# Kernel tuning notes

Measured on AMD Instinct MI355X. Metric: run time of the kernel, lower is better.

The kernel has to match this reference:

```python
import jax, jax.numpy as jnp
import numpy as np

B, S, Hd = 2, 2048, 2048
NH, DH = 16, 128
FF = 4 * Hd
EPS = 1e-5


def layer_norm(x, g, b):
    mu = jnp.mean(x, axis=-1, keepdims=True)
    var = jnp.mean(jnp.square(x - mu), axis=-1, keepdims=True)
    return (x - mu) * jax.lax.rsqrt(var + EPS) * g + b


def setup_inputs() -> dict:
    key = jax.random.key(0)
    ks = jax.random.split(key, 10)
    s = lambda n: 1.0 / np.sqrt(n)
    return {
        "hidden_states": jax.random.normal(ks[0], (B, S, Hd), jnp.float32),
        "attention_mask": jnp.zeros((B, S), jnp.float32),
        "ln1_g": jnp.ones((Hd,), jnp.float32),
        "ln1_b": jnp.zeros((Hd,), jnp.float32),
        "ln2_g": jnp.ones((Hd,), jnp.float32),
        "ln2_b": jnp.zeros((Hd,), jnp.float32),
        "Wq": jax.random.normal(ks[1], (Hd, NH * DH), jnp.float32) * s(Hd),
        "Wk": jax.random.normal(ks[2], (Hd, NH * DH), jnp.float32) * s(Hd),
        "Wv": jax.random.normal(ks[3], (Hd, NH * DH), jnp.float32) * s(Hd),
        "Wo": jax.random.normal(ks[4], (NH * DH, Hd), jnp.float32) * s(NH * DH),
        "W1": jax.random.normal(ks[5], (Hd, FF), jnp.float32) * s(Hd),
        "b1": jnp.zeros((FF,), jnp.float32),
        "W2": jax.random.normal(ks[6], (FF, Hd), jnp.float32) * s(FF),
        "b2": jnp.zeros((Hd,), jnp.float32),
    }


def reference(hidden_states, attention_mask, ln1_g, ln1_b, ln2_g, ln2_b,
              Wq, Wk, Wv, Wo, W1, b1, W2, b2):
    x = hidden_states
    # --- attention sub-block ---
    h = layer_norm(x, ln1_g, ln1_b)
    q = (h @ Wq).reshape(B, S, NH, DH)
    k = (h @ Wk).reshape(B, S, NH, DH)
    v = (h @ Wv).reshape(B, S, NH, DH)
    scores = jnp.einsum("bqhd,bkhd->bhqk", q, k) / np.sqrt(DH).astype(np.float32)
    scores = scores + attention_mask[:, None, None, :]  # additive mask
    probs = jax.nn.softmax(scores, axis=-1)
    ctx = jnp.einsum("bhqk,bkhd->bqhd", probs, v).reshape(B, S, NH * DH)
    x = x + ctx @ Wo
    # --- MLP sub-block ---
    h = layer_norm(x, ln2_g, ln2_b)
    h = jax.nn.gelu(h @ W1 + b1, approximate=False)
    x = x + h @ W2 + b2
    return x
```

## Files before the change

### kernel.cpp

```cpp
#include <hip/hip_runtime.h>
#include <math.h>

#define B_ 2
#define S_ 2048
#define HD 2048
#define NH_ 16
#define DH_ 128
#define FF_ 8192
#define MROWS (B_*S_)
#define LDQ 6144

typedef __attribute__((ext_vector_type(8))) short bf16x8;
typedef __attribute__((ext_vector_type(4))) short s16x4;
typedef __attribute__((ext_vector_type(4))) float f32x4;

static __device__ __forceinline__ unsigned short f2bf(float f) {
    unsigned u = __float_as_uint(f);
    u += 0x7fffu + ((u >> 16) & 1u);
    return (unsigned short)(u >> 16);
}

static __device__ __forceinline__ void gload_lds16(const void* g, void* lds) {
    __builtin_amdgcn_global_load_lds((const __attribute__((address_space(1))) void*)g,
                                     (__attribute__((address_space(3))) void*)lds, 16, 0, 0);
}

__global__ __launch_bounds__(256) void trcvt_kernel(const float* __restrict__ W,
        short* __restrict__ Wt, int K, int N) {
    __shared__ float tile[32][33];
    int t = threadIdx.x;
    int tx = t & 31, ty = t >> 5;
    int r0 = blockIdx.y * 32, c0 = blockIdx.x * 32;
    #pragma unroll
    for (int i = 0; i < 4; i++)
        tile[ty + 8*i][tx] = W[(size_t)(r0 + ty + 8*i) * N + c0 + tx];
    __syncthreads();
    #pragma unroll
    for (int i = 0; i < 4; i++)
        Wt[(size_t)(c0 + ty + 8*i) * K + r0 + tx] = (short)f2bf(tile[tx][ty + 8*i]);
}

__global__ __launch_bounds__(256) void vtrans_kernel(const short* __restrict__ qkv,
        short* __restrict__ vT) {
    __shared__ short tile[32][33];
    int t = threadIdx.x;
    int tx = t & 31, ty = t >> 5;
    int c0 = blockIdx.x * 32;
    int r0 = blockIdx.y * 32;
    int b  = blockIdx.z;
    #pragma unroll
    for (int i = 0; i < 4; i++)
        tile[ty + 8*i][tx] = qkv[(size_t)(b*S_ + r0 + ty + 8*i) * LDQ + 4096 + c0 + tx];
    __syncthreads();
    #pragma unroll
    for (int i = 0; i < 4; i++)
        vT[((size_t)(c0 + ty + 8*i) * 2 + b) * S_ + r0 + tx] = tile[tx][ty + 8*i];
}

__global__ __launch_bounds__(256) void ln_kernel(const float* __restrict__ x,
                const float* __restrict__ g, const float* __restrict__ b,
                short* __restrict__ out) {
    int row = blockIdx.x;
    const float* xr = x + (size_t)row * HD;
    short* orow = out + (size_t)row * HD;
    int t = threadIdx.x;

    float4 v0 = ((const float4*)xr)[t];
    float4 v1 = ((const float4*)xr)[t + 256];
    float s  = v0.x + v0.y + v0.z + v0.w + v1.x + v1.y + v1.z + v1.w;
    float ss = v0.x*v0.x + v0.y*v0.y + v0.z*v0.z + v0.w*v0.w
             + v1.x*v1.x + v1.y*v1.y + v1.z*v1.z + v1.w*v1.w;

    #pragma unroll
    for (int off = 1; off < 64; off <<= 1) {
        s  += __shfl_xor(s,  off, 64);
        ss += __shfl_xor(ss, off, 64);
    }
    __shared__ float ws_s[4], ws_q[4];
    int wid = t >> 6;
    if ((t & 63) == 0) { ws_s[wid] = s; ws_q[wid] = ss; }
    __syncthreads();
    s  = ws_s[0] + ws_s[1] + ws_s[2] + ws_s[3];
    ss = ws_q[0] + ws_q[1] + ws_q[2] + ws_q[3];

    float mu  = s * (1.0f / HD);
    float var = ss * (1.0f / HD) - mu * mu;
    float rs  = rsqrtf(var + 1e-5f);

    float4 g0 = ((const float4*)g)[t];
    float4 g1 = ((const float4*)g)[t + 256];
    float4 b0 = ((const float4*)b)[t];
    float4 b1 = ((const float4*)b)[t + 256];
    s16x4 o0, o1;
    o0.x = (short)f2bf((v0.x - mu) * rs * g0.x + b0.x);
    o0.y = (short)f2bf((v0.y - mu) * rs * g0.y + b0.y);
    o0.z = (short)f2bf((v0.z - mu) * rs * g0.z + b0.z);
    o0.w = (short)f2bf((v0.w - mu) * rs * g0.w + b0.w);
    o1.x = (short)f2bf((v1.x - mu) * rs * g1.x + b1.x);
    o1.y = (short)f2bf((v1.y - mu) * rs * g1.y + b1.y);
    o1.z = (short)f2bf((v1.z - mu) * rs * g1.z + b1.z);
    o1.w = (short)f2bf((v1.w - mu) * rs * g1.w + b1.w);
    ((s16x4*)orow)[t]       = o0;
    ((s16x4*)orow)[t + 256] = o1;
}

#define CKPRO() { if constexpr (BM == 256) asm volatile("s_waitcnt vmcnt(4)" ::: "memory"); \
                  else                     asm volatile("s_waitcnt vmcnt(3)" ::: "memory"); }
#define CKLOOP() { if constexpr (BM == 256) asm volatile("s_waitcnt vmcnt(8)" ::: "memory"); \
                   else                     asm volatile("s_waitcnt vmcnt(6)" ::: "memory"); }

#define GPH(BUF, KK, STG) {                                                       \
    bf16x8 av[MFR];                                                               \
    _Pragma("unroll") for (int f = 0; f < MFR; f++)                               \
        av[f] = *(const bf16x8*)(pA + (BUF)*ABUF + (KK)*AKK + f*1024);            \
    bf16x8 bv[4];                                                                 \
    _Pragma("unroll") for (int n = 0; n < 4; n++)                                 \
        bv[n] = *(const bf16x8*)(pB + (BUF)*BBUF + (KK)*BKK + n*1024);            \
    STG;                                                                          \
    CKLOOP();                                                                     \
    __builtin_amdgcn_s_barrier();                                                 \
    __builtin_amdgcn_s_setprio(1);                                                \
    _Pragma("unroll") for (int f = 0; f < MFR; f++)                               \
        _Pragma("unroll") for (int n = 0; n < 4; n++)                             \
            acc[f][n] = __builtin_amdgcn_mfma_f32_16x16x32_bf16(                  \
                av[f], bv[n], acc[f][n], 0, 0, 0);                                \
    __builtin_amdgcn_s_setprio(0);                                                \
    __builtin_amdgcn_s_barrier();                                                 \
}

template<int BM, bool OUTBF16, bool BIAS, bool RES, bool GELU>
__global__ __launch_bounds__(512, 2) void gemm256(
        const short* __restrict__ A, const short* __restrict__ Bt,
        const float* __restrict__ bias, const float* __restrict__ res,
        void* __restrict__ Cout, int M, int N, int K) {
    constexpr int MFR  = BM / 32;
    constexpr int LA   = BM / 128;
    constexpr int AKK  = BM * 64;
    constexpr int ABUF = 2 * AKK;
    constexpr int BKK  = 256 * 64;
    constexpr int BBUF = 2 * BKK;
    __shared__ __align__(16) char ldsA[2 * ABUF];
    __shared__ __align__(16) char ldsB[2 * BBUF];

    int tid = threadIdx.x;
    int wave = tid >> 6, lane = tid & 63;
    int l4 = lane >> 4, lm = lane & 15;
    int wm = wave >> 2, wn = wave & 3;

    int nx = N >> 8;
    int bid = blockIdx.x;
    int m0, n0;
    if constexpr (BM == 128) {
        int xcd = bid & 7, local = bid >> 3;
        int mt = (xcd & 3) * 8 + (local >> 2);
        int ntt = (xcd >> 2) * 4 + (local & 3);
        m0 = mt * 128; n0 = ntt << 8;
    } else {
        m0 = (bid / nx) * BM; n0 = (bid % nx) << 8;
    }

    const short* Atile = A + (size_t)m0 * K;
    const short* Btile = Bt + (size_t)n0 * K;
    const int NT = K >> 6;

    int slot = (l4 ^ (lm & 3) ^ (lm >> 2)) & 3;
    const char* pA = ldsA + (wm * (BM/2) + lm) * 64 + slot * 16;
    const char* pB = ldsB + (wn * 64 + lm) * 64 + slot * 16;

    auto stageA = [&](int t, int kh, int buf) {
        int tw = (t >= NT) ? t - NT : t;
        const short* g = Atile + tw * 64 + kh * 32;
        char* dst = ldsA + buf * ABUF + kh * AKK;
        #pragma unroll
        for (int s = 0; s < LA; s++) {
            int n = wave * (64 * LA) + s * 64 + lane;
            int row = n >> 2, c = n & 3;
            int cs = (c ^ (row & 3) ^ ((row >> 2) & 3)) & 3;
            gload_lds16(g + (size_t)row * K + cs * 8, dst + n * 16);
        }
    };
    auto stageB = [&](int t, int kh, int buf) {
        int tw = (t >= NT) ? t - NT : t;
        const short* g = Btile + tw * 64 + kh * 32;
        char* dst = ldsB + buf * BBUF + kh * BKK;
        #pragma unroll
        for (int s = 0; s < 2; s++) {
            int n = wave * 128 + s * 64 + lane;
            int row = n >> 2, c = n & 3;
            int cs = (c ^ (row & 3) ^ ((row >> 2) & 3)) & 3;
            gload_lds16(g + (size_t)row * K + cs * 8, dst + n * 16);
        }
    };

    f32x4 acc[MFR][4] = {};

    stageA(0, 0, 0); stageB(0, 0, 0);
    stageA(0, 1, 0); stageB(0, 1, 0);
    stageA(1, 0, 1); stageB(1, 0, 1);
    CKPRO();
    __builtin_amdgcn_s_barrier();

    const int NITER = NT >> 1;
    for (int j = 0; j < NITER; j++) {
        int T = 2 * j;
        GPH(0, 0, { stageA(T+1, 1, 1); stageB(T+1, 1, 1); });
        GPH(0, 1, { stageA(T+2, 0, 0); stageB(T+2, 0, 0); });
        GPH(1, 0, { stageA(T+2, 1, 0); stageB(T+2, 1, 0); });
        GPH(1, 1, { stageA(T+3, 0, 1); stageB(T+3, 0, 1); });
    }
    asm volatile("s_waitcnt vmcnt(0)" ::: "memory");
    __builtin_amdgcn_s_barrier();

    #pragma unroll
    for (int n = 0; n < 4; n++) {
        int colb = n0 + wn * 64 + n * 16 + lm;
        float bvs = BIAS ? bias[colb] : 0.f;
        #pragma unroll
        for (int m = 0; m < MFR; m++) {
            #pragma unroll
            for (int r = 0; r < 4; r++) {
                int row = m0 + wm * (BM/2) + m * 16 + l4 * 4 + r;
                float v = acc[m][n][r] + bvs;
                if (GELU) v = 0.5f * v * (1.0f + erff(v * 0.70710678118654752f));
                size_t off = (size_t)row * N + colb;
                if (RES) v += res[off];
                if (OUTBF16) ((short*)Cout)[off] = (short)f2bf(v);
                else         ((float*)Cout)[off] = v;
            }
        }
    }
}

__global__ __launch_bounds__(256) void attn_kernel(
        const short* __restrict__ qkv, const short* __restrict__ vT,
        const float* __restrict__ mask, short* __restrict__ ctx) {
    __shared__ __align__(16) short Ks[64*128];
    __shared__ __align__(16) short Vt[128*64];
    __shared__ __align__(16) short Ps[4][16*72];
    int t = threadIdx.x;
    int wave = t >> 6, lane = t & 63;
    int l4 = lane >> 4, lm = lane & 15;
    int q0 = blockIdx.x * 64, h = blockIdx.y, zb = blockIdx.z;
    const float scale = 0.08838834764831845f;

    bf16x8 aq[4];
    {
        const short* qrow = qkv + (size_t)(zb*S_ + q0 + wave*16 + lm) * LDQ + h*DH_;
        #pragma unroll
        for (int ks = 0; ks < 4; ks++)
            aq[ks] = *(const bf16x8*)(qrow + ks*32 + l4*8);
    }

    float m_r[4], l_r[4];
    #pragma unroll
    for (int r = 0; r < 4; r++) { m_r[r] = -INFINITY; l_r[r] = 0.f; }
    f32x4 o[8];
    #pragma unroll
    for (int i = 0; i < 8; i++) o[i] = (f32x4){0.f, 0.f, 0.f, 0.f};

    for (int kv0 = 0; kv0 < S_; kv0 += 64) {
        __syncthreads();
        #pragma unroll
        for (int L = 0; L < 4; L++) {
            int c = (wave*4 + L)*64 + lane;
            int krow = c >> 4, kc = c & 15;
            int ksrc = (kc & 8) | ((kc ^ (krow & 7)) & 7);
            gload_lds16(qkv + (size_t)(zb*S_ + kv0 + krow)*LDQ + 2048 + h*DH_ + ksrc*8,
                        (char*)Ks + c*16);
            int drow = c >> 3, dc = c & 7;
            int dsrc = dc ^ (drow & 7);
            gload_lds16(vT + ((size_t)(h*DH_ + drow)*2 + zb)*S_ + kv0 + dsrc*8,
                        (char*)Vt + c*16);
        }
        __syncthreads();

        f32x4 s[4];
        #pragma unroll
        for (int nb = 0; nb < 4; nb++) s[nb] = (f32x4){0.f, 0.f, 0.f, 0.f};
        __builtin_amdgcn_s_setprio(1);
        #pragma unroll
        for (int nb = 0; nb < 4; nb++) {
            int row = nb*16 + lm;
            #pragma unroll
            for (int ks = 0; ks < 4; ks++) {
                bf16x8 bk = *(const bf16x8*)((const char*)Ks +
                              ((row*256 + ks*64 + l4*16) ^ ((row & 7) << 4)));
                s[nb] = __builtin_amdgcn_mfma_f32_16x16x32_bf16(aq[ks], bk, s[nb], 0, 0, 0);
            }
        }
        __builtin_amdgcn_s_setprio(0);

        float mk[4];
        #pragma unroll
        for (int nb = 0; nb < 4; nb++) mk[nb] = mask[(size_t)zb*S_ + kv0 + nb*16 + lm];

        float pv_[4][4], fac[4];
        #pragma unroll
        for (int r = 0; r < 4; r++) {
            float vmax = -INFINITY;
            #pragma unroll
            for (int nb = 0; nb < 4; nb++) {
                float v = s[nb][r] * scale + mk[nb];
                pv_[r][nb] = v;
                vmax = fmaxf(vmax, v);
            }
            vmax = fmaxf(vmax, __shfl_xor(vmax, 1, 64));
            vmax = fmaxf(vmax, __shfl_xor(vmax, 2, 64));
            vmax = fmaxf(vmax, __shfl_xor(vmax, 4, 64));
            vmax = fmaxf(vmax, __shfl_xor(vmax, 8, 64));
            float nm = fmaxf(m_r[r], vmax);
            fac[r] = __expf(m_r[r] - nm);
            float ps = 0.f;
            #pragma unroll
            for (int nb = 0; nb < 4; nb++) {
                float e = __expf(pv_[r][nb] - nm);
                pv_[r][nb] = e;
                ps += e;
            }
            ps += __shfl_xor(ps, 1, 64);
            ps += __shfl_xor(ps, 2, 64);
            ps += __shfl_xor(ps, 4, 64);
            ps += __shfl_xor(ps, 8, 64);
            l_r[r] = l_r[r] * fac[r] + ps;
            m_r[r] = nm;
        }
        #pragma unroll
        for (int i = 0; i < 8; i++)
            #pragma unroll
            for (int r = 0; r < 4; r++) o[i][r] *= fac[r];

        short* Pw = (short*)Ps[wave];
        #pragma unroll
        for (int r = 0; r < 4; r++)
            #pragma unroll
            for (int nb = 0; nb < 4; nb++)
                Pw[(l4*4 + r)*72 + nb*16 + lm] = (short)f2bf(pv_[r][nb]);

        __builtin_amdgcn_s_setprio(1);
        #pragma unroll
        for (int ks = 0; ks < 2; ks++) {
            bf16x8 ap = *(const bf16x8*)(Pw + lm*72 + ks*32 + l4*8);
            #pragma unroll
            for (int nd = 0; nd < 8; nd++) {
                int d = nd*16 + lm;
                bf16x8 bvv = *(const bf16x8*)((const char*)Vt +
                              (((d*128) + ks*64 + l4*16) ^ ((d & 7) << 4)));
                o[nd] = __builtin_amdgcn_mfma_f32_16x16x32_bf16(ap, bvv, o[nd], 0, 0, 0);
            }
        }
        __builtin_amdgcn_s_setprio(0);
    }

    float inv[4];
    #pragma unroll
    for (int r = 0; r < 4; r++) inv[r] = 1.0f / l_r[r];
    #pragma unroll
    for (int nd = 0; nd < 8; nd++) {
        #pragma unroll
        for (int r = 0; r < 4; r++) {
            size_t row = (size_t)(zb*S_ + q0 + wave*16 + l4*4 + r);
            ctx[row * HD + h*DH_ + nd*16 + lm] = (short)f2bf(o[nd][r] * inv[r]);
        }
    }
}

extern "C" void kernel_launch(void* const* d_in, const int* in_sizes, int n_in,
                              void* d_out, int out_size, void* d_ws, size_t ws_size,
                              hipStream_t stream) {
    const float* x      = (const float*)d_in[0];
    const float* mask   = (const float*)d_in[1];
    const float* ln1_g  = (const float*)d_in[2];
    const float* ln1_b  = (const float*)d_in[3];
    const float* ln2_g  = (const float*)d_in[4];
    const float* ln2_b  = (const float*)d_in[5];
    const float* Wq     = (const float*)d_in[6];
    const float* Wk     = (const float*)d_in[7];
    const float* Wv     = (const float*)d_in[8];
    const float* Wo     = (const float*)d_in[9];
    const float* W1     = (const float*)d_in[10];
    const float* b1     = (const float*)d_in[11];
    const float* W2     = (const float*)d_in[12];
    const float* b2     = (const float*)d_in[13];
    float* out = (float*)d_out;

    char* ws = (char*)d_ws;
    size_t off = 0;
    const size_t WSQ  = (size_t)HD * HD * 2;
    const size_t WFF  = (size_t)HD * FF_ * 2;
    const size_t ACTB = (size_t)MROWS * HD * 2;
    short* WqkvT = (short*)(ws + off); off += 3 * WSQ;
    short* WoT   = (short*)(ws + off); off += WSQ;
    short* W1T   = (short*)(ws + off); off += WFF;
    short* W2T   = (short*)(ws + off); off += WFF;
    short* hb    = (short*)(ws + off); off += ACTB;
    short* qkv   = (short*)(ws + off); off += (size_t)MROWS * LDQ * 2;
    short* vTb   = (short*)(ws + off); off += (size_t)HD * B_ * S_ * 2;
    float* x1    = (float*)(ws + off); off += (size_t)MROWS * HD * 4;
    short* cb    = WqkvT;
    short* act   = qkv;

    dim3 blk(256);

    trcvt_kernel<<<dim3(HD/32,  HD/32),  blk, 0, stream>>>(Wq, WqkvT,                 HD, HD);
    trcvt_kernel<<<dim3(HD/32,  HD/32),  blk, 0, stream>>>(Wk, WqkvT + (size_t)HD*HD, HD, HD);
    trcvt_kernel<<<dim3(HD/32,  HD/32),  blk, 0, stream>>>(Wv, WqkvT + (size_t)2*HD*HD, HD, HD);
    trcvt_kernel<<<dim3(HD/32,  HD/32),  blk, 0, stream>>>(Wo, WoT, HD, HD);
    trcvt_kernel<<<dim3(FF_/32, HD/32),  blk, 0, stream>>>(W1, W1T, HD, FF_);
    trcvt_kernel<<<dim3(HD/32,  FF_/32), blk, 0, stream>>>(W2, W2T, FF_, HD);

    ln_kernel<<<MROWS, blk, 0, stream>>>(x, ln1_g, ln1_b, hb);

    gemm256<256,true,false,false,false><<<dim3((MROWS/256)*(LDQ/256)), 512, 0, stream>>>(
        hb, WqkvT, nullptr, nullptr, qkv, MROWS, LDQ, HD);

    vtrans_kernel<<<dim3(HD/32, S_/32, B_), blk, 0, stream>>>(qkv, vTb);

    attn_kernel<<<dim3(S_/64, NH_, B_), blk, 0, stream>>>(qkv, vTb, mask, cb);

    gemm256<128,false,false,true,false><<<dim3((MROWS/128)*(HD/256)), 512, 0, stream>>>(
        cb, WoT, nullptr, x, x1, MROWS, HD, HD);

    ln_kernel<<<MROWS, blk, 0, stream>>>(x1, ln2_g, ln2_b, hb);

    gemm256<256,true,true,false,true><<<dim3((MROWS/256)*(FF_/256)), 512, 0, stream>>>(
        hb, W1T, b1, nullptr, act, MROWS, FF_, HD);

    gemm256<128,false,true,true,false><<<dim3((MROWS/128)*(HD/256)), 512, 0, stream>>>(
        act, W2T, b2, x1, out, MROWS, HD, FF_);
}
```

Measured before the change: 833.7 us.

## Add 128x128 double-buffered bf16 GEMM kernel for QKV and W1 projections

New measurement: 798.8 us. 4.2% less time.

```diff
diff --git a/kernel.cpp b/kernel.cpp
--- a/kernel.cpp
+++ b/kernel.cpp
@@ -102,6 +102,100 @@
     o1.w = (short)f2bf((v1.w - mu) * rs * g1.w + b1.w);
     ((s16x4*)orow)[t]       = o0;
     ((s16x4*)orow)[t + 256] = o1;
+}
+
+template<bool OUTBF16, bool BIAS, bool RES, bool GELU>
+__global__ __launch_bounds__(256, 2) void gemm128(
+        const short* __restrict__ A, const short* __restrict__ Bt,
+        const float* __restrict__ bias, const float* __restrict__ res,
+        void* __restrict__ Cout, int M, int N, int K) {
+    __shared__ __align__(16) char ldsA[2][128 * 128];
+    __shared__ __align__(16) char ldsB[2][128 * 128];
+
+    int tid = threadIdx.x;
+    int wave = tid >> 6, lane = tid & 63;
+    int l4 = lane >> 4, lm = lane & 15;
+    int wm = wave >> 1, wn = wave & 1;
+
+    int nx = N >> 7;
+    int bid = blockIdx.x;
+    int m0 = (bid / nx) * 128, n0 = (bid % nx) << 7;
+
+    const short* Atile = A + (size_t)m0 * K;
+    const short* Btile = Bt + (size_t)n0 * K;
+    const int NT = K >> 6;
+
+    auto stage = [&](int t, int buf) {
+        int tw = (t >= NT) ? t - NT : t;
+        const short* gA = Atile + tw * 64;
+        const short* gB = Btile + tw * 64;
+        #pragma unroll
+        for (int s = 0; s < 4; s++) {
+            int n = (wave * 4 + s) * 64 + lane;
+            int row = n >> 3, c = n & 7;
+            int cs = c ^ (row & 7);
+            gload_lds16(gA + (size_t)row * K + cs * 8, ldsA[buf] + n * 16);
+            gload_lds16(gB + (size_t)row * K + cs * 8, ldsB[buf] + n * 16);
+        }
+    };
+
+    int ch0 = (l4) ^ (lm & 7);
+    int ch1 = (4 | l4) ^ (lm & 7);
+    const char* pA = (const char*)ldsA + (wm * 64 + lm) * 128;
+    const char* pB = (const char*)ldsB + (wn * 64 + lm) * 128;
+
+    f32x4 acc[4][4] = {};
+
+    stage(0, 0);
+    for (int t = 0; t < NT; t++) {
+        int buf = t & 1;
+        stage(t + 1, buf ^ 1);
+        asm volatile("s_waitcnt vmcnt(8)" ::: "memory");
+        __builtin_amdgcn_s_barrier();
+        __builtin_amdgcn_sched_barrier(0);
+        size_t bo = (size_t)buf * 128 * 128;
+        __builtin_amdgcn_s_setprio(1);
+        #pragma unroll
+        for (int kk = 0; kk < 2; kk++) {
+            int ch = kk ? ch1 : ch0;
+            bf16x8 av[4], bv[4];
+            #pragma unroll
+            for (int f = 0; f < 4; f++)
+                av[f] = *(const bf16x8*)(pA + bo + f * 2048 + ch * 16);
+            #pragma unroll
+            for (int nn = 0; nn < 4; nn++)
+                bv[nn] = *(const bf16x8*)(pB + bo + nn * 2048 + ch * 16);
+            #pragma unroll
+            for (int f = 0; f < 4; f++)
+                #pragma unroll
+                for (int nn = 0; nn < 4; nn++)
+                    acc[f][nn] = __builtin_amdgcn_mfma_f32_16x16x32_bf16(
+                        av[f], bv[nn], acc[f][nn], 0, 0, 0);
+        }
+        __builtin_amdgcn_s_setprio(0);
+        __builtin_amdgcn_s_barrier();
+    }
+    asm volatile("s_waitcnt vmcnt(0)" ::: "memory");
+    __builtin_amdgcn_s_barrier();
+
+    #pragma unroll
+    for (int nn = 0; nn < 4; nn++) {
+        int colb = n0 + wn * 64 + nn * 16 + lm;
+        float bvs = BIAS ? bias[colb] : 0.f;
+        #pragma unroll
+        for (int m = 0; m < 4; m++) {
+            #pragma unroll
+            for (int r = 0; r < 4; r++) {
+                int row = m0 + wm * 64 + m * 16 + l4 * 4 + r;
+                float v = acc[m][nn][r] + bvs;
+                if (GELU) v = 0.5f * v * (1.0f + erff(v * 0.70710678118654752f));
+                size_t off = (size_t)row * N + colb;
+                if (RES) v += res[off];
+                if (OUTBF16) ((short*)Cout)[off] = (short)f2bf(v);
+                else         ((float*)Cout)[off] = v;
+            }
+        }
+    }
 }
 
 #define CKPRO() { if constexpr (BM == 256) asm volatile("s_waitcnt vmcnt(4)" ::: "memory"); \
@@ -410,7 +504,7 @@
 
     ln_kernel<<<MROWS, blk, 0, stream>>>(x, ln1_g, ln1_b, hb);
 
-    gemm256<256,true,false,false,false><<<dim3((MROWS/256)*(LDQ/256)), 512, 0, stream>>>(
+    gemm128<true,false,false,false><<<dim3((MROWS/128)*(LDQ/128)), 256, 0, stream>>>(
         hb, WqkvT, nullptr, nullptr, qkv, MROWS, LDQ, HD);
 
     vtrans_kernel<<<dim3(HD/32, S_/32, B_), blk, 0, stream>>>(qkv, vTb);
@@ -422,7 +516,7 @@
 
     ln_kernel<<<MROWS, blk, 0, stream>>>(x1, ln2_g, ln2_b, hb);
 
-    gemm256<256,true,true,false,true><<<dim3((MROWS/256)*(FF_/256)), 512, 0, stream>>>(
+    gemm128<true,true,false,true><<<dim3((MROWS/128)*(FF_/128)), 256, 0, stream>>>(
         hb, W1T, b1, nullptr, act, MROWS, FF_, HD);
 
     gemm256<128,false,true,true,false><<<dim3((MROWS/128)*(HD/256)), 512, 0, stream>>>(
```
